# Kernel tuning notes

Hardware: AMD Instinct MI355X
Metric: run time of the kernel (lower is better)

Reference implementation:

```python
import jax, jax.numpy as jnp
import numpy as np

B, A, M = 8, 200_000, 64


def calc_iou(a, b):
    # a: [A,4] anchors, b: [M,4] gt boxes (x1,y1,x2,y2)
    area_b = (b[:, 2] - b[:, 0]) * (b[:, 3] - b[:, 1])            # [M]
    iw = jnp.clip(jnp.minimum(a[:, 2:3], b[:, 2]) - jnp.maximum(a[:, 0:1], b[:, 0]), 0.0)
    ih = jnp.clip(jnp.minimum(a[:, 3:4], b[:, 3]) - jnp.maximum(a[:, 1:2], b[:, 1]), 0.0)
    area_a = ((a[:, 2] - a[:, 0]) * (a[:, 3] - a[:, 1]))[:, None]  # [A,1]
    inter = iw * ih                                                # [A,M]
    ua = jnp.clip(area_a + area_b - inter, 1e-8)
    return inter / ua


def setup_inputs() -> dict:
    key = jax.random.key(0)
    k1, k2, k3, k4, k5, k6, k7, k8 = jax.random.split(key, 8)
    classifications = jax.random.normal(k1, (B, A, 2), dtype=jnp.float32)
    bbox_regressions = jax.random.normal(k2, (B, A, 4), dtype=jnp.float32) * 0.1
    # realistic anchor boxes over a 640x640 image
    cx = jax.random.uniform(k3, (A,), minval=0.0, maxval=640.0)
    cy = jax.random.uniform(k4, (A,), minval=0.0, maxval=640.0)
    wh = jax.random.uniform(k5, (A, 2), minval=8.0, maxval=128.0)
    anchor = jnp.stack([cx - wh[:, 0] / 2, cy - wh[:, 1] / 2,
                        cx + wh[:, 0] / 2, cy + wh[:, 1] / 2], axis=1)
    anchors = anchor[None]  # [1,A,4]
    # GT boxes sampled near anchors so positives (IoU>=0.5) actually occur
    idx = jax.random.randint(k6, (B, M), 0, A)
    ann = anchor[idx] + jax.random.normal(k7, (B, M, 4)) * 1.5
    invalid = jax.random.uniform(k8, (B, M)) < 0.25
    x1 = jnp.where(invalid, -1.0, jnp.maximum(ann[..., 0], 0.5))
    ann = ann.at[..., 0].set(x1)
    return {"classifications": classifications, "bbox_regressions": bbox_regressions,
            "anchors": anchors, "annotations": ann.astype(jnp.float32)}


BOX_STD = jnp.array([0.1, 0.1, 0.2, 0.2], dtype=jnp.float32)


def _forward(classifications, bbox_regressions, anchors, annotations):
    anchor = anchors[0]
    aw = anchor[:, 2] - anchor[:, 0]
    ah = anchor[:, 3] - anchor[:, 1]
    acx = anchor[:, 0] + 0.5 * aw
    acy = anchor[:, 1] + 0.5 * ah
    ar = jnp.arange(A)

    def per_image(cls, reg, ann):
        valid = ann[:, 0] > 0                      # [M] (torch filters these rows out)
        boxes = ann[:, :4]
        iou = calc_iou(anchor, boxes)              # [A,M]
        iou = jnp.where(valid[None, :], iou, -1.0)  # invalid GT never matched
        iou_max = jnp.max(iou, axis=1)
        iou_arg = jnp.argmax(iou, axis=1)
        pos = iou_max >= 0.5
        neg = iou_max < 0.3
        num_pos = jnp.sum(pos)
        num_neg = jnp.sum(neg)
        keep = num_pos * 3
        eff = jnp.minimum(keep, num_neg)           # torch truncates sorted losses to keep
        # hard negative mining: sort -cls[:,1] over negatives, descending
        neg_l = jnp.where(neg, -cls[:, 1], -jnp.inf)
        sorted_neg = -jnp.sort(-neg_l)             # descending, -inf last
        sel = ar < eff
        efff = jnp.maximum(eff, 1).astype(cls.dtype)
        neg_mean = jnp.sum(jnp.where(sel, sorted_neg, 0.0)) / efff
        nposf = jnp.maximum(num_pos, 1).astype(cls.dtype)
        pos_mean = jnp.sum(jnp.where(pos, -cls[:, 0], 0.0)) / nposf
        cls_loss = jnp.where(num_pos > 0, pos_mean + neg_mean, 0.0)
        ag = boxes[iou_arg]                        # [A,4] assigned GT per anchor
        gw = ag[:, 2] - ag[:, 0]
        gh = ag[:, 3] - ag[:, 1]
        gcx = ag[:, 0] + 0.5 * gw
        gcy = ag[:, 1] + 0.5 * gh
        dx = (gcx - acx) / (aw + 1e-14)
        dy = (gcy - acy) / (ah + 1e-14)
        dw = jnp.log(jnp.where(pos, gw / aw, 1.0))  # guard log for non-positive rows
        dh = jnp.log(jnp.where(pos, gh / ah, 1.0))
        targets = jnp.stack([dx, dy, dw, dh], axis=1) / BOX_STD  # [A,4]
        d = jnp.abs(targets - reg)
        sl = jnp.where(d < 1.0, 0.5 * d * d, d - 0.5)  # SmoothL1, beta=1
        denom = jnp.maximum(num_pos * 4, 1).astype(cls.dtype)
        box_loss = jnp.sum(jnp.where(pos[:, None], sl, 0.0)) / denom
        box_loss = jnp.where(num_pos > 0, box_loss, 0.0)
        return cls_loss, box_loss

    cls_losses, box_losses = jax.vmap(per_image)(classifications, bbox_regressions, annotations)
    return cls_losses, box_losses


def reference(classifications, bbox_regressions, anchors, annotations):
    return _forward(classifications, bbox_regressions, anchors, annotations)
```

## Files before the change

### kernel.cpp

```cpp
#include <hip/hip_runtime.h>
#include <stdint.h>

#define NA 200000
#define NB 8
#define NM 64
#define APB 1024
#define CPB 196
#define NA4 50000
#define SPB 128
#define SEGCAP 25600
#define IMGCAP (8*SEGCAP)
#define C2CAP 6144

#define O_SCAL 0
#define O_L1C  128
#define O_L1S  2176
#define O_GH4K 4224
#define O_KEYS 36992
#define O_CBUF 1636992
#define N_ZERO 36992

__device__ __forceinline__ unsigned int f2key(float f) {
    unsigned int u = __float_as_uint(f);
    return (u & 0x80000000u) ? ~u : (u | 0x80000000u);
}
__device__ __forceinline__ float key2f(unsigned int k) {
    return (k & 0x80000000u) ? __uint_as_float(k & 0x7fffffffu) : __uint_as_float(~k);
}
__device__ __forceinline__ unsigned int calck(const unsigned int* scal, int b) {
    const unsigned int np = scal[b * 16], nn = scal[b * 16 + 1];
    if (!np) return 0u;
    const unsigned int kp = np * 3u;
    return (kp < nn) ? kp : nn;
}

__device__ __forceinline__ void wave_sel256(
    const unsigned int* __restrict__ cnt, const float* __restrict__ sum,
    unsigned int target, unsigned int* c, unsigned int* cab, float* sab)
{
    const int lane = (int)(threadIdx.x & 63u);
    const uint4  c4 = ((const uint4*)cnt)[lane];
    const float4 s4 = ((const float4*)sum)[lane];
    unsigned int S = c4.x + c4.y + c4.z + c4.w;
    float Sf = s4.x + s4.y + s4.z + s4.w;
    for (int d = 1; d < 64; d <<= 1) {
        const unsigned int oc = __shfl_down(S, d);
        const float of = __shfl_down(Sf, d);
        if (lane + d < 64) { S += oc; Sf += of; }
    }
    unsigned int Sn = __shfl_down(S, 1);
    float Sfn = __shfl_down(Sf, 1);
    if (lane == 63) { Sn = 0u; Sfn = 0.0f; }
    const unsigned int cb[4] = {c4.x, c4.y, c4.z, c4.w};
    const float sb[4] = {s4.x, s4.y, s4.z, s4.w};
    unsigned int run = Sn; float runs = Sfn;
    bool found = false; unsigned int lc = 0, lcab = 0; float lsab = 0.0f;
#pragma unroll
    for (int j = 3; j >= 0; --j) {
        const unsigned int prev = run; const float prevs = runs;
        run += cb[j]; runs += sb[j];
        if (run >= target && prev < target) {
            found = true; lc = (unsigned int)(4 * lane + j); lcab = prev; lsab = prevs;
        }
    }
    const unsigned long long m = __ballot(found);
    const int src = __ffsll((long long)m) - 1;
    *c = __shfl(lc, src); *cab = __shfl(lcab, src); *sab = __shfl(lsab, src);
}

__device__ __forceinline__ void wave_sel4096_cnt(
    const unsigned int* hc, unsigned int target, unsigned int* bin, unsigned int* cab)
{
    const int lane = (int)(threadIdx.x & 63u);
    unsigned int cs = 0;
    const uint4* p = (const uint4*)(hc + lane * 64);
#pragma unroll
    for (int j = 0; j < 16; ++j) { const uint4 u = p[j]; cs += u.x + u.y + u.z + u.w; }
    unsigned int S = cs;
    for (int d = 1; d < 64; d <<= 1) { const unsigned int o = __shfl_down(S, d); if (lane + d < 64) S += o; }
    unsigned int Sn = __shfl_down(S, 1); if (lane == 63) Sn = 0u;
    const bool f1 = (S >= target) && (Sn < target);
    const unsigned long long m1 = __ballot(f1);
    const int chunk = __ffsll((long long)m1) - 1;
    const unsigned int above = __shfl(Sn, chunk);
    unsigned int S2 = hc[chunk * 64 + lane];
    for (int d = 1; d < 64; d <<= 1) { const unsigned int o = __shfl_down(S2, d); if (lane + d < 64) S2 += o; }
    unsigned int S2n = __shfl_down(S2, 1); if (lane == 63) S2n = 0u;
    const bool f2 = (above + S2 >= target) && (above + S2n < target);
    const unsigned long long m2 = __ballot(f2);
    const int l2 = __ffsll((long long)m2) - 1;
    *bin = (unsigned int)(chunk * 64 + l2);
    *cab = above + __shfl(S2n, l2);
}

__device__ __forceinline__ void iou_upd(
    const float4 Aq, const float aaq, const float4 B, const float abj, const int j,
    float& bi, float& bu, int& arg)
{
#pragma clang fp contract(off)
    const float iw = fmaxf(fminf(Aq.z, B.z) - fmaxf(Aq.x, B.x), 0.0f);
    const float ih = fmaxf(fminf(Aq.w, B.w) - fmaxf(Aq.y, B.y), 0.0f);
    const float inter = iw * ih;
    const float ua = fmaxf(aaq + abj - inter, 1e-8f);
    if (inter * bu > bi * ua) { bi = inter; bu = ua; arg = j; }
}

__device__ __forceinline__ void epi2(
    int b, int i, float4 a4, int arg, bool pos, bool neg, float2 cv,
    const float* __restrict__ reg, const float4* sbox, unsigned int* __restrict__ keys,
    unsigned int* hc8, float* hs8, float& posv, float& boxv)
{
    unsigned int key = 0u;
    if (neg) {
        const float nl = -cv.y;
        key = f2key(nl);
        atomicAdd(&hc8[key >> 24], 1u);
        atomicAdd(&hs8[key >> 24], nl);
    }
    keys[(size_t)b * NA + i] = key;
    if (pos) {
        posv += -cv.x;
        const float4 g = sbox[arg];
        const float aw = a4.z - a4.x, ah = a4.w - a4.y;
        const float acx = a4.x + 0.5f * aw, acy = a4.y + 0.5f * ah;
        const float gw = g.z - g.x, gh = g.w - g.y;
        const float gcx = g.x + 0.5f * gw, gcy = g.y + 0.5f * gh;
        const float t0 = ((gcx - acx) / (aw + 1e-14f)) / 0.1f;
        const float t1 = ((gcy - acy) / (ah + 1e-14f)) / 0.1f;
        const float t2 = logf(gw / aw) / 0.2f;
        const float t3 = logf(gh / ah) / 0.2f;
        const float4 r = ((const float4*)reg)[(size_t)b * NA + i];
        const float d0 = fabsf(t0 - r.x);
        const float d1 = fabsf(t1 - r.y);
        const float d2 = fabsf(t2 - r.z);
        const float d3 = fabsf(t3 - r.w);
        const float l0 = (d0 < 1.0f) ? 0.5f * d0 * d0 : d0 - 0.5f;
        const float l1 = (d1 < 1.0f) ? 0.5f * d1 * d1 : d1 - 0.5f;
        const float l2 = (d2 < 1.0f) ? 0.5f * d2 * d2 : d2 - 0.5f;
        const float l3 = (d3 < 1.0f) ? 0.5f * d3 * d3 : d3 - 0.5f;
        boxv += l0 + l1 + l2 + l3;
    }
}

__global__ __launch_bounds__(256, 4) void k_main(
    const float* __restrict__ cls, const float* __restrict__ reg,
    const float* __restrict__ anchors, const float* __restrict__ ann,
    unsigned int* __restrict__ scal, unsigned int* __restrict__ l1cnt,
    float* __restrict__ l1sum, unsigned int* __restrict__ keys)
{
    __shared__ float4 sbox[NM];
    __shared__ unsigned int s_nv;
    __shared__ unsigned int hc8[256];
    __shared__ float hs8[256];
    __shared__ unsigned int s_np, s_nn;
    __shared__ float s_ps, s_bs;

    const int b = blockIdx.y;
    const int tid = threadIdx.x;
    const int ibase = blockIdx.x * APB + tid;

    float4 A[4]; float2 CV[4];
#pragma unroll
    for (int q = 0; q < 4; ++q) {
        const int i = ibase + q * 256;
        if (i < NA) {
            A[q]  = ((const float4*)anchors)[i];
            CV[q] = ((const float2*)cls)[(size_t)b * NA + i];
        } else {
            A[q]  = make_float4(0.f, 0.f, 0.f, 0.f);
            CV[q] = make_float2(0.f, 0.f);
        }
    }

    if (tid < NM) {
        const float4 bb = ((const float4*)ann)[b * NM + tid];
        const bool valid = (bb.x > 0.0f);
        const unsigned long long m = __ballot(valid);
        if (valid) {
            const int p = __popcll(m & ((1ull << (tid & 63)) - 1ull));
            sbox[p] = bb;
        }
        if (tid == 0) s_nv = (unsigned int)__popcll(m);
    }
    hc8[tid] = 0u; hs8[tid] = 0.0f;
    if (tid == 0) { s_np = 0u; s_nn = 0u; s_ps = 0.0f; s_bs = 0.0f; }
    __syncthreads();
    const int nv = (int)s_nv;
    const int nvr = (nv + 3) & ~3;
    if (tid >= nv && tid < nvr) {
        sbox[tid] = make_float4(__builtin_inff(), __builtin_inff(),
                                -__builtin_inff(), -__builtin_inff());
    }
    __syncthreads();

    float aa[4];
    {
#pragma clang fp contract(off)
#pragma unroll
        for (int q = 0; q < 4; ++q) aa[q] = (A[q].z - A[q].x) * (A[q].w - A[q].y);
    }
    float bi[4] = {-1.0f, -1.0f, -1.0f, -1.0f};
    float bu[4] = {1.0f, 1.0f, 1.0f, 1.0f};
    int arg[4] = {0, 0, 0, 0};

#pragma unroll 1
    for (int mo = 0; mo < nvr; mo += 4) {
        const float4 b0 = sbox[mo + 0];
        const float4 b1 = sbox[mo + 1];
        const float4 b2 = sbox[mo + 2];
        const float4 b3 = sbox[mo + 3];
        float ab0, ab1, ab2, ab3;
        {
#pragma clang fp contract(off)
            ab0 = (b0.z - b0.x) * (b0.w - b0.y);
            ab1 = (b1.z - b1.x) * (b1.w - b1.y);
            ab2 = (b2.z - b2.x) * (b2.w - b2.y);
            ab3 = (b3.z - b3.x) * (b3.w - b3.y);
        }
#pragma unroll
        for (int q = 0; q < 4; ++q) {
            iou_upd(A[q], aa[q], b0, ab0, mo + 0, bi[q], bu[q], arg[q]);
            iou_upd(A[q], aa[q], b1, ab1, mo + 1, bi[q], bu[q], arg[q]);
            iou_upd(A[q], aa[q], b2, ab2, mo + 2, bi[q], bu[q], arg[q]);
            iou_upd(A[q], aa[q], b3, ab3, mo + 3, bi[q], bu[q], arg[q]);
        }
    }

    bool pos[4], neg[4];
    {
#pragma clang fp contract(off)
#pragma unroll
        for (int q = 0; q < 4; ++q) {
            pos[q] = (bi[q] >= 0.5f * bu[q]);
            neg[q] = (bi[q] < 0.3f * bu[q]);
        }
    }

    float posv = 0.0f, boxv = 0.0f;
#pragma unroll
    for (int q = 0; q < 4; ++q) {
        const int i = ibase + q * 256;
        if (i < NA) {
            epi2(b, i, A[q], arg[q], pos[q], neg[q], CV[q], reg, sbox, keys, hc8, hs8, posv, boxv);
        } else { pos[q] = false; neg[q] = false; }
    }

    unsigned int pc = 0, nc = 0; bool anyp = false;
#pragma unroll
    for (int q = 0; q < 4; ++q) {
        const unsigned long long pb = __ballot(pos[q]);
        const unsigned long long nb = __ballot(neg[q]);
        anyp |= (pb != 0ull);
        pc += (unsigned int)__popcll(pb);
        nc += (unsigned int)__popcll(nb);
    }
    if (anyp) {
        for (int off = 32; off; off >>= 1) {
            posv += __shfl_xor(posv, off);
            boxv += __shfl_xor(boxv, off);
        }
    }
    if ((tid & 63) == 0) {
        if (nc) atomicAdd(&s_nn, nc);
        if (pc) { atomicAdd(&s_np, pc); atomicAdd(&s_ps, posv); atomicAdd(&s_bs, boxv); }
    }
    __syncthreads();
    unsigned int* sg = scal + b * 16;
    if (tid == 0) {
        if (s_nn) atomicAdd(&sg[1], s_nn);
        if (s_np) {
            atomicAdd(&sg[0], s_np);
            atomicAdd((float*)(sg + 2), s_ps);
            atomicAdd((float*)(sg + 3), s_bs);
        }
    }
    if (hc8[tid]) {
        atomicAdd(&l1cnt[b * 256 + tid], hc8[tid]);
        atomicAdd(&l1sum[b * 256 + tid], hs8[tid]);
    }
}

__global__ __launch_bounds__(256) void k_h2c(
    const unsigned int* __restrict__ keys, unsigned int* __restrict__ scal,
    const unsigned int* __restrict__ l1c, const float* __restrict__ l1s,
    unsigned int* __restrict__ cbuf, unsigned int* __restrict__ gh4k)
{
    __shared__ unsigned int wcnt[4];
    __shared__ unsigned int sbase;
    const int b = blockIdx.x >> 7;
    const int sub = blockIdx.x & (SPB - 1);
    const int tid = threadIdx.x;
    const unsigned int k = calck(scal, b);
    if (k == 0) return;
    unsigned int c1, cab1; float sab1;
    wave_sel256(l1c + b * 256, l1s + b * 256, k, &c1, &cab1, &sab1);

    const uint4* kp4 = (const uint4*)(keys + (size_t)b * NA);
    const int j0 = sub * 256 + tid;
    const int j1 = j0 + SPB * 256;
    const uint4 v0 = kp4[j0];
    const uint4 v1 = (j1 < NA4) ? kp4[j1] : make_uint4(0, 0, 0, 0);
    const unsigned int kk[8] = {v0.x, v0.y, v0.z, v0.w, v1.x, v1.y, v1.z, v1.w};

    unsigned int* gh = gh4k + b * 4096;
    const int lane = tid & 63;
    const int wave = tid >> 6;
    bool m[8];
    unsigned long long mask[8];
    unsigned int tot = 0;
#pragma unroll
    for (int j = 0; j < 8; ++j) {
        m[j] = kk[j] && (kk[j] >> 24) == c1;
        mask[j] = __ballot(m[j]);
        tot += (unsigned int)__popcll(mask[j]);
        if (m[j]) atomicAdd(&gh[(kk[j] >> 12) & 0xfffu], 1u);
    }
    if (lane == 0) wcnt[wave] = tot;
    __syncthreads();
    if (tid == 0) {
        unsigned int p = 0;
#pragma unroll
        for (int w = 0; w < 4; ++w) { const unsigned int t = wcnt[w]; wcnt[w] = p; p += t; }
        sbase = p ? atomicAdd(&scal[b * 16 + 8 + (sub & 7)], p) : 0u;
    }
    __syncthreads();
    unsigned int base = sbase + wcnt[wave];
    if (tot) {
        unsigned int* cb = cbuf + (size_t)b * IMGCAP + (sub & 7) * SEGCAP;
        const unsigned long long lt = (lane == 63) ? ~0ull >> 1 : ((1ull << (lane + 1)) - 1ull) >> 1;
#pragma unroll
        for (int j = 0; j < 8; ++j) {
            if (m[j]) cb[base + (unsigned int)__popcll(mask[j] & lt)] = kk[j];
            base += (unsigned int)__popcll(mask[j]);
        }
    }
}

__global__ __launch_bounds__(1024) void k_fin2(
    const unsigned int* __restrict__ scal,
    const unsigned int* __restrict__ l1c, const float* __restrict__ l1s,
    const unsigned int* __restrict__ cbuf, const unsigned int* __restrict__ gh4k,
    float* __restrict__ out)
{
    __shared__ unsigned int hc[4096];
    __shared__ unsigned int s_sel[2];
    __shared__ float spart[16];
    __shared__ unsigned int s_cnt;
    __shared__ unsigned int cbin[C2CAP];

    const int b = blockIdx.x;
    const int tid = threadIdx.x;
    const unsigned int np = scal[b * 16];
    const unsigned int k = calck(scal, b);
    float s_top = 0.0f;

    if (k > 0) {
        unsigned int c1, cab1; float sab1;
        wave_sel256(l1c + b * 256, l1s + b * 256, k, &c1, &cab1, &sab1);
        const unsigned int t2 = k - cab1;
        unsigned int ns[8];
#pragma unroll
        for (int s = 0; s < 8; ++s) ns[s] = scal[b * 16 + 8 + s];

        for (int j = tid; j < 4096; j += 1024) hc[j] = gh4k[b * 4096 + j];
        if (tid == 0) s_cnt = 0u;
        __syncthreads();
        if (tid < 64) {
            unsigned int c2w, cab2w;
            wave_sel4096_cnt(hc, t2, &c2w, &cab2w);
            if (tid == 0) { s_sel[0] = c2w; s_sel[1] = cab2w; }
        }
        __syncthreads();
        const unsigned int c2 = s_sel[0];
        const unsigned int t3 = t2 - s_sel[1];
        for (int j = tid; j < 4096; j += 1024) hc[j] = 0u;
        __syncthreads();

        float ls = 0.0f;
#pragma unroll 1
        for (int s = 0; s < 8; ++s) {
            const unsigned int n2 = ns[s];
            const unsigned int* cb = cbuf + (size_t)b * IMGCAP + s * SEGCAP;
            for (unsigned int base = 0; base < n2; base += 4096) {
                const unsigned int i0 = base + tid, i1 = i0 + 1024, i2 = i0 + 2048, i3 = i0 + 3072;
                const unsigned int k0 = (i0 < n2) ? cb[i0] : 0u;
                const unsigned int k1 = (i1 < n2) ? cb[i1] : 0u;
                const unsigned int k2 = (i2 < n2) ? cb[i2] : 0u;
                const unsigned int k3 = (i3 < n2) ? cb[i3] : 0u;
                const unsigned int kk4[4] = {k0, k1, k2, k3};
#pragma unroll
                for (int j = 0; j < 4; ++j) {
                    const unsigned int kj = kk4[j];
                    const unsigned int mid = (kj >> 12) & 0xfffu;
                    if (mid > c2) ls += key2f(kj);
                    else if (kj && mid == c2) {
                        const unsigned int idx = atomicAdd(&s_cnt, 1u);
                        if (idx < C2CAP) cbin[idx] = kj;
                        atomicAdd(&hc[kj & 0xfffu], 1u);
                    }
                }
            }
        }
        __syncthreads();
        if (tid < 64) {
            unsigned int c3w, cab3w;
            wave_sel4096_cnt(hc, t3, &c3w, &cab3w);
            if (tid == 0) { s_sel[0] = c3w; s_sel[1] = cab3w; }
        }
        __syncthreads();
        const unsigned int c3 = s_sel[0];
        const unsigned int keyv = (c1 << 24) | (c2 << 12) | c3;
        const unsigned int rem = t3 - s_sel[1];
        const float v = key2f(keyv);
        const unsigned int cnt2 = s_cnt;

        if (cnt2 <= C2CAP) {
            for (unsigned int i = tid; i < cnt2; i += 1024) {
                const unsigned int kj = cbin[i];
                if ((kj & 0xfffu) > c3) ls += key2f(kj);
            }
        } else {
#pragma unroll 1
            for (int s = 0; s < 8; ++s) {
                const unsigned int n2 = ns[s];
                const unsigned int* cb = cbuf + (size_t)b * IMGCAP + s * SEGCAP;
                for (unsigned int base = 0; base < n2; base += 4096) {
                    const unsigned int i0 = base + tid, i1 = i0 + 1024, i2 = i0 + 2048, i3 = i0 + 3072;
                    const unsigned int k0 = (i0 < n2) ? cb[i0] : 0u;
                    const unsigned int k1 = (i1 < n2) ? cb[i1] : 0u;
                    const unsigned int k2 = (i2 < n2) ? cb[i2] : 0u;
                    const unsigned int k3 = (i3 < n2) ? cb[i3] : 0u;
                    if (k0 && ((k0 >> 12) & 0xfffu) == c2 && (k0 & 0xfffu) > c3) ls += key2f(k0);
                    if (k1 && ((k1 >> 12) & 0xfffu) == c2 && (k1 & 0xfffu) > c3) ls += key2f(k1);
                    if (k2 && ((k2 >> 12) & 0xfffu) == c2 && (k2 & 0xfffu) > c3) ls += key2f(k2);
                    if (k3 && ((k3 >> 12) & 0xfffu) == c2 && (k3 & 0xfffu) > c3) ls += key2f(k3);
                }
            }
        }

        for (int off = 32; off; off >>= 1) ls += __shfl_xor(ls, off);
        if ((tid & 63) == 0) spart[tid >> 6] = ls;
        __syncthreads();
        if (tid == 0) {
            float S = 0.0f;
#pragma unroll
            for (int w = 0; w < 16; ++w) S += spart[w];
            s_top = sab1 + S + (float)rem * v;
        }
    }

    if (tid == 0) {
        float cls_loss = 0.0f, box_loss = 0.0f;
        if (np > 0) {
            const float* fsc = (const float*)(scal + b * 16);
            const float pos_mean = fsc[2] / (float)np;
            const float neg_mean = s_top / (float)((k > 0) ? k : 1u);
            cls_loss = pos_mean + neg_mean;
            box_loss = fsc[3] / (float)(4u * np);
        }
        out[b] = cls_loss;
        out[NB + b] = box_loss;
    }
}

extern "C" void kernel_launch(void* const* d_in, const int* in_sizes, int n_in,
                              void* d_out, int out_size, void* d_ws, size_t ws_size,
                              hipStream_t stream) {
    const float* cls     = (const float*)d_in[0];
    const float* reg     = (const float*)d_in[1];
    const float* anchors = (const float*)d_in[2];
    const float* ann     = (const float*)d_in[3];
    unsigned int* ws = (unsigned int*)d_ws;
    unsigned int* scal = ws + O_SCAL;
    unsigned int* l1c  = ws + O_L1C;   float* l1s = (float*)(ws + O_L1S);
    unsigned int* gh4k = ws + O_GH4K;
    unsigned int* keys = ws + O_KEYS;
    unsigned int* cbuf = ws + O_CBUF;
    (void)in_sizes; (void)n_in; (void)out_size; (void)ws_size;

    hipMemsetAsync(d_ws, 0, (size_t)N_ZERO * 4, stream);
    k_main<<<dim3(CPB, NB),  256,  0, stream>>>(cls, reg, anchors, ann, scal, l1c, l1s, keys);
    k_h2c <<<dim3(NB * SPB), 256,  0, stream>>>(keys, scal, l1c, l1s, cbuf, gh4k);
    k_fin2<<<dim3(NB),       1024, 0, stream>>>(scal, l1c, l1s, cbuf, gh4k, (float*)d_out);
}
```

Measured before the change: 178.3 us.

## Fuse radix-select tail into one kernel with per-bin key lists and last-block finish

The compaction and final-selection kernels are merged into one kernel. It builds global per-bin counts and sums for the second radix level, stores keys into fixed-capacity per-bin lists with an overflow buffer, and lets the last block to finish for each image do the final selection. This removes a kernel launch and replaces the rescans of a compacted buffer with a small per-bin list read plus precomputed bin sums. The trade-off is heavy global atomic contention on the count and sum arrays, a larger zeroed workspace, and a slow full-key fallback path when the overflow buffer fills.

Measured after the change: 313.3 us. 75.8% more time.

```diff
diff --git a/kernel.cpp b/kernel.cpp
--- a/kernel.cpp
+++ b/kernel.cpp
@@ -8,17 +8,18 @@
 #define CPB 196
 #define NA4 50000
 #define SPB 128
-#define SEGCAP 25600
-#define IMGCAP (8*SEGCAP)
-#define C2CAP 6144
+#define CAP 32
+#define OVFCAP 32768
 
 #define O_SCAL 0
 #define O_L1C  128
 #define O_L1S  2176
-#define O_GH4K 4224
-#define O_KEYS 36992
-#define O_CBUF 1636992
-#define N_ZERO 36992
+#define O_GCNT 4224
+#define O_GSUM 36992
+#define N_ZERO 69760
+#define O_KEYS 69760
+#define O_BINL 1669760
+#define O_OVF  2718336
 
 __device__ __forceinline__ unsigned int f2key(float f) {
     unsigned int u = __float_as_uint(f);
@@ -91,6 +92,49 @@
     const int l2 = __ffsll((long long)m2) - 1;
     *bin = (unsigned int)(chunk * 64 + l2);
     *cab = above + __shfl(S2n, l2);
+}
+
+__device__ __forceinline__ void wave_sel4096_cs(
+    const unsigned int* hc, const float* hs, unsigned int target,
+    unsigned int* bin, unsigned int* cab, float* sab)
+{
+    const int lane = (int)(threadIdx.x & 63u);
+    unsigned int cs = 0; float fs = 0.0f;
+    const uint4*  p = (const uint4*)(hc + lane * 64);
+    const float4* q = (const float4*)(hs + lane * 64);
+#pragma unroll
+    for (int j = 0; j < 16; ++j) {
+        const uint4 u = p[j];  cs += u.x + u.y + u.z + u.w;
+        const float4 f = q[j]; fs += f.x + f.y + f.z + f.w;
+    }
+    unsigned int S = cs; float F = fs;
+    for (int d = 1; d < 64; d <<= 1) {
+        const unsigned int o = __shfl_down(S, d);
+        const float of = __shfl_down(F, d);
+        if (lane + d < 64) { S += o; F += of; }
+    }
+    unsigned int Sn = __shfl_down(S, 1); float Fn = __shfl_down(F, 1);
+    if (lane == 63) { Sn = 0u; Fn = 0.0f; }
+    const bool f1 = (S >= target) && (Sn < target);
+    const unsigned long long m1 = __ballot(f1);
+    const int chunk = __ffsll((long long)m1) - 1;
+    const unsigned int above = __shfl(Sn, chunk);
+    const float fabove = __shfl(Fn, chunk);
+    unsigned int S2 = hc[chunk * 64 + lane];
+    float F2 = hs[chunk * 64 + lane];
+    for (int d = 1; d < 64; d <<= 1) {
+        const unsigned int o = __shfl_down(S2, d);
+        const float of = __shfl_down(F2, d);
+        if (lane + d < 64) { S2 += o; F2 += of; }
+    }
+    unsigned int S2n = __shfl_down(S2, 1); float F2n = __shfl_down(F2, 1);
+    if (lane == 63) { S2n = 0u; F2n = 0.0f; }
+    const bool f2 = (above + S2 >= target) && (above + S2n < target);
+    const unsigned long long m2 = __ballot(f2);
+    const int l2 = __ffsll((long long)m2) - 1;
+    *bin = (unsigned int)(chunk * 64 + l2);
+    *cab = above + __shfl(S2n, l2);
+    *sab = fabove + __shfl(F2n, l2);
 }
 
 __device__ __forceinline__ void iou_upd(
@@ -241,7 +285,7 @@
     for (int q = 0; q < 4; ++q) {
         const int i = ibase + q * 256;
         if (i < NA) {
-            epi2(b, i, A[q], arg[q], pos[q], neg[q], CV[q], reg, sbox, keys, hc8, hs8, posv, boxv);
+            epi2(b, i, A[q], arg[q], pos[q], neg[q], CV[q], reg, (const float4*)sbox, keys, hc8, hs8, posv, boxv);
         } else { pos[q] = false; neg[q] = false; }
     }
 
@@ -280,125 +324,102 @@
     }
 }
 
-__global__ __launch_bounds__(256) void k_h2c(
+__global__ __launch_bounds__(256) void k_tail(
     const unsigned int* __restrict__ keys, unsigned int* __restrict__ scal,
     const unsigned int* __restrict__ l1c, const float* __restrict__ l1s,
-    unsigned int* __restrict__ cbuf, unsigned int* __restrict__ gh4k)
-{
-    __shared__ unsigned int wcnt[4];
-    __shared__ unsigned int sbase;
-    const int b = blockIdx.x >> 7;
+    unsigned int* __restrict__ gcnt, float* __restrict__ gsum,
+    unsigned int* __restrict__ binl, unsigned int* __restrict__ ovf,
+    float* __restrict__ out)
+{
+    __shared__ unsigned int hc[4096];
+    __shared__ float hs[4096];
+    __shared__ unsigned int s_last;
+    __shared__ unsigned int s_sel[2];
+    __shared__ float s_fs;
+    __shared__ float spart[4];
+
+    const int b   = blockIdx.x >> 7;
     const int sub = blockIdx.x & (SPB - 1);
     const int tid = threadIdx.x;
     const unsigned int k = calck(scal, b);
-    if (k == 0) return;
-    unsigned int c1, cab1; float sab1;
-    wave_sel256(l1c + b * 256, l1s + b * 256, k, &c1, &cab1, &sab1);
-
-    const uint4* kp4 = (const uint4*)(keys + (size_t)b * NA);
-    const int j0 = sub * 256 + tid;
-    const int j1 = j0 + SPB * 256;
-    const uint4 v0 = kp4[j0];
-    const uint4 v1 = (j1 < NA4) ? kp4[j1] : make_uint4(0, 0, 0, 0);
-    const unsigned int kk[8] = {v0.x, v0.y, v0.z, v0.w, v1.x, v1.y, v1.z, v1.w};
-
-    unsigned int* gh = gh4k + b * 4096;
-    const int lane = tid & 63;
-    const int wave = tid >> 6;
-    bool m[8];
-    unsigned long long mask[8];
-    unsigned int tot = 0;
-#pragma unroll
-    for (int j = 0; j < 8; ++j) {
-        m[j] = kk[j] && (kk[j] >> 24) == c1;
-        mask[j] = __ballot(m[j]);
-        tot += (unsigned int)__popcll(mask[j]);
-        if (m[j]) atomicAdd(&gh[(kk[j] >> 12) & 0xfffu], 1u);
-    }
-    if (lane == 0) wcnt[wave] = tot;
+
+    if (k) {
+        unsigned int c1, cab1; float sab1;
+        wave_sel256(l1c + b * 256, l1s + b * 256, k, &c1, &cab1, &sab1);
+        const uint4* kp4 = (const uint4*)(keys + (size_t)b * NA);
+        const int j0 = sub * 256 + tid;
+        const int j1 = j0 + SPB * 256;
+        const uint4 v0 = kp4[j0];
+        const uint4 v1 = (j1 < NA4) ? kp4[j1] : make_uint4(0, 0, 0, 0);
+        const unsigned int kk[8] = {v0.x, v0.y, v0.z, v0.w, v1.x, v1.y, v1.z, v1.w};
+#pragma unroll
+        for (int j = 0; j < 8; ++j) {
+            const unsigned int kj = kk[j];
+            if (kj && (kj >> 24) == c1) {
+                const unsigned int mid = (kj >> 12) & 0xfffu;
+                const unsigned int gi = ((unsigned int)b << 12) + mid;
+                const unsigned int slot = atomicAdd(&gcnt[gi], 1u);
+                atomicAdd(&gsum[gi], key2f(kj));
+                if (slot < CAP) binl[gi * CAP + slot] = kj;
+                else {
+                    const unsigned int o = atomicAdd(&scal[b * 16 + 4], 1u);
+                    if (o < OVFCAP) ovf[b * OVFCAP + o] = kj;
+                }
+            }
+        }
+    }
+
+    __threadfence();
+    if (tid == 0) {
+        const unsigned int d = atomicAdd(&scal[b * 16 + 5], 1u);
+        s_last = (d == SPB - 1) ? 1u : 0u;
+    }
     __syncthreads();
-    if (tid == 0) {
-        unsigned int p = 0;
-#pragma unroll
-        for (int w = 0; w < 4; ++w) { const unsigned int t = wcnt[w]; wcnt[w] = p; p += t; }
-        sbase = p ? atomicAdd(&scal[b * 16 + 8 + (sub & 7)], p) : 0u;
-    }
-    __syncthreads();
-    unsigned int base = sbase + wcnt[wave];
-    if (tot) {
-        unsigned int* cb = cbuf + (size_t)b * IMGCAP + (sub & 7) * SEGCAP;
-        const unsigned long long lt = (lane == 63) ? ~0ull >> 1 : ((1ull << (lane + 1)) - 1ull) >> 1;
-#pragma unroll
-        for (int j = 0; j < 8; ++j) {
-            if (m[j]) cb[base + (unsigned int)__popcll(mask[j] & lt)] = kk[j];
-            base += (unsigned int)__popcll(mask[j]);
-        }
-    }
-}
-
-__global__ __launch_bounds__(1024) void k_fin2(
-    const unsigned int* __restrict__ scal,
-    const unsigned int* __restrict__ l1c, const float* __restrict__ l1s,
-    const unsigned int* __restrict__ cbuf, const unsigned int* __restrict__ gh4k,
-    float* __restrict__ out)
-{
-    __shared__ unsigned int hc[4096];
-    __shared__ unsigned int s_sel[2];
-    __shared__ float spart[16];
-    __shared__ unsigned int s_cnt;
-    __shared__ unsigned int cbin[C2CAP];
-
-    const int b = blockIdx.x;
-    const int tid = threadIdx.x;
+    if (!s_last) return;
+    __threadfence();
+
     const unsigned int np = scal[b * 16];
-    const unsigned int k = calck(scal, b);
     float s_top = 0.0f;
-
-    if (k > 0) {
+    if (k) {
         unsigned int c1, cab1; float sab1;
         wave_sel256(l1c + b * 256, l1s + b * 256, k, &c1, &cab1, &sab1);
         const unsigned int t2 = k - cab1;
-        unsigned int ns[8];
-#pragma unroll
-        for (int s = 0; s < 8; ++s) ns[s] = scal[b * 16 + 8 + s];
-
-        for (int j = tid; j < 4096; j += 1024) hc[j] = gh4k[b * 4096 + j];
-        if (tid == 0) s_cnt = 0u;
+        for (int j = tid; j < 4096; j += 256) {
+            hc[j] = gcnt[((unsigned int)b << 12) + j];
+            hs[j] = gsum[((unsigned int)b << 12) + j];
+        }
         __syncthreads();
         if (tid < 64) {
-            unsigned int c2w, cab2w;
-            wave_sel4096_cnt(hc, t2, &c2w, &cab2w);
-            if (tid == 0) { s_sel[0] = c2w; s_sel[1] = cab2w; }
+            unsigned int c2w, cab2w; float sab2w;
+            wave_sel4096_cs(hc, hs, t2, &c2w, &cab2w, &sab2w);
+            if (tid == 0) { s_sel[0] = c2w; s_sel[1] = cab2w; s_fs = sab2w; }
         }
         __syncthreads();
         const unsigned int c2 = s_sel[0];
         const unsigned int t3 = t2 - s_sel[1];
-        for (int j = tid; j < 4096; j += 1024) hc[j] = 0u;
-        __syncthreads();
-
-        float ls = 0.0f;
-#pragma unroll 1
-        for (int s = 0; s < 8; ++s) {
-            const unsigned int n2 = ns[s];
-            const unsigned int* cb = cbuf + (size_t)b * IMGCAP + s * SEGCAP;
-            for (unsigned int base = 0; base < n2; base += 4096) {
-                const unsigned int i0 = base + tid, i1 = i0 + 1024, i2 = i0 + 2048, i3 = i0 + 3072;
-                const unsigned int k0 = (i0 < n2) ? cb[i0] : 0u;
-                const unsigned int k1 = (i1 < n2) ? cb[i1] : 0u;
-                const unsigned int k2 = (i2 < n2) ? cb[i2] : 0u;
-                const unsigned int k3 = (i3 < n2) ? cb[i3] : 0u;
-                const unsigned int kk4[4] = {k0, k1, k2, k3};
-#pragma unroll
-                for (int j = 0; j < 4; ++j) {
-                    const unsigned int kj = kk4[j];
-                    const unsigned int mid = (kj >> 12) & 0xfffu;
-                    if (mid > c2) ls += key2f(kj);
-                    else if (kj && mid == c2) {
-                        const unsigned int idx = atomicAdd(&s_cnt, 1u);
-                        if (idx < C2CAP) cbin[idx] = kj;
-                        atomicAdd(&hc[kj & 0xfffu], 1u);
-                    }
-                }
+        const float sab2 = s_fs;
+        const unsigned int nbin = hc[c2];
+        __syncthreads();
+        for (int j = tid; j < 4096; j += 256) hc[j] = 0u;
+        __syncthreads();
+
+        const unsigned int oc = scal[b * 16 + 4];
+        const bool fb = (oc > OVFCAP);
+        const unsigned int nb2 = (nbin < CAP) ? nbin : CAP;
+        const unsigned int bbase = (((unsigned int)b << 12) + c2) * CAP;
+
+        if (!fb) {
+            for (unsigned int i = tid; i < nb2; i += 256)
+                atomicAdd(&hc[binl[bbase + i] & 0xfffu], 1u);
+            for (unsigned int i = tid; i < oc; i += 256) {
+                const unsigned int kj = ovf[b * OVFCAP + i];
+                if (((kj >> 12) & 0xfffu) == c2) atomicAdd(&hc[kj & 0xfffu], 1u);
+            }
+        } else {
+            for (unsigned int i = tid; i < NA; i += 256) {
+                const unsigned int kj = keys[(size_t)b * NA + i];
+                if (kj && (kj >> 24) == c1 && ((kj >> 12) & 0xfffu) == c2)
+                    atomicAdd(&hc[kj & 0xfffu], 1u);
             }
         }
         __syncthreads();
@@ -409,44 +430,32 @@
         }
         __syncthreads();
         const unsigned int c3 = s_sel[0];
+        const unsigned int rem = t3 - s_sel[1];
         const unsigned int keyv = (c1 << 24) | (c2 << 12) | c3;
-        const unsigned int rem = t3 - s_sel[1];
         const float v = key2f(keyv);
-        const unsigned int cnt2 = s_cnt;
-
-        if (cnt2 <= C2CAP) {
-            for (unsigned int i = tid; i < cnt2; i += 1024) {
-                const unsigned int kj = cbin[i];
+
+        float ls = 0.0f;
+        if (!fb) {
+            for (unsigned int i = tid; i < nb2; i += 256) {
+                const unsigned int kj = binl[bbase + i];
                 if ((kj & 0xfffu) > c3) ls += key2f(kj);
             }
+            for (unsigned int i = tid; i < oc; i += 256) {
+                const unsigned int kj = ovf[b * OVFCAP + i];
+                if (((kj >> 12) & 0xfffu) == c2 && (kj & 0xfffu) > c3) ls += key2f(kj);
+            }
         } else {
-#pragma unroll 1
-            for (int s = 0; s < 8; ++s) {
-                const unsigned int n2 = ns[s];
-                const unsigned int* cb = cbuf + (size_t)b * IMGCAP + s * SEGCAP;
-                for (unsigned int base = 0; base < n2; base += 4096) {
-                    const unsigned int i0 = base + tid, i1 = i0 + 1024, i2 = i0 + 2048, i3 = i0 + 3072;
-                    const unsigned int k0 = (i0 < n2) ? cb[i0] : 0u;
-                    const unsigned int k1 = (i1 < n2) ? cb[i1] : 0u;
-                    const unsigned int k2 = (i2 < n2) ? cb[i2] : 0u;
-                    const unsigned int k3 = (i3 < n2) ? cb[i3] : 0u;
-                    if (k0 && ((k0 >> 12) & 0xfffu) == c2 && (k0 & 0xfffu) > c3) ls += key2f(k0);
-                    if (k1 && ((k1 >> 12) & 0xfffu) == c2 && (k1 & 0xfffu) > c3) ls += key2f(k1);
-                    if (k2 && ((k2 >> 12) & 0xfffu) == c2 && (k2 & 0xfffu) > c3) ls += key2f(k2);
-                    if (k3 && ((k3 >> 12) & 0xfffu) == c2 && (k3 & 0xfffu) > c3) ls += key2f(k3);
-                }
-            }
-        }
-
+            for (unsigned int i = tid; i < NA; i += 256) {
+                const unsigned int kj = keys[(size_t)b * NA + i];
+                if (kj && (kj >> 24) == c1 && ((kj >> 12) & 0xfffu) == c2 && (kj & 0xfffu) > c3)
+                    ls += key2f(kj);
+            }
+        }
         for (int off = 32; off; off >>= 1) ls += __shfl_xor(ls, off);
         if ((tid & 63) == 0) spart[tid >> 6] = ls;
         __syncthreads();
-        if (tid == 0) {
-            float S = 0.0f;
-#pragma unroll
-            for (int w = 0; w < 16; ++w) S += spart[w];
-            s_top = sab1 + S + (float)rem * v;
-        }
+        if (tid == 0)
+            s_top = sab1 + sab2 + (spart[0] + spart[1] + spart[2] + spart[3]) + (float)rem * v;
     }
 
     if (tid == 0) {
@@ -472,14 +481,15 @@
     const float* ann     = (const float*)d_in[3];
     unsigned int* ws = (unsigned int*)d_ws;
     unsigned int* scal = ws + O_SCAL;
-    unsigned int* l1c  = ws + O_L1C;   float* l1s = (float*)(ws + O_L1S);
-    unsigned int* gh4k = ws + O_GH4K;
+    unsigned int* l1c  = ws + O_L1C;   float* l1s  = (float*)(ws + O_L1S);
+    unsigned int* gcnt = ws + O_GCNT;  float* gsum = (float*)(ws + O_GSUM);
     unsigned int* keys = ws + O_KEYS;
-    unsigned int* cbuf = ws + O_CBUF;
+    unsigned int* binl = ws + O_BINL;
+    unsigned int* ovf  = ws + O_OVF;
     (void)in_sizes; (void)n_in; (void)out_size; (void)ws_size;
 
     hipMemsetAsync(d_ws, 0, (size_t)N_ZERO * 4, stream);
-    k_main<<<dim3(CPB, NB),  256,  0, stream>>>(cls, reg, anchors, ann, scal, l1c, l1s, keys);
-    k_h2c <<<dim3(NB * SPB), 256,  0, stream>>>(keys, scal, l1c, l1s, cbuf, gh4k);
-    k_fin2<<<dim3(NB),       1024, 0, stream>>>(scal, l1c, l1s, cbuf, gh4k, (float*)d_out);
-}
+    k_main<<<dim3(CPB, NB),  256, 0, stream>>>(cls, reg, anchors, ann, scal, l1c, l1s, keys);
+    k_tail<<<dim3(NB * SPB), 256, 0, stream>>>(keys, scal, l1c, l1s, gcnt, gsum, binl, ovf,
+                                               (float*)d_out);
+}
```
